# Kernel optimization log

Hardware: AMD Instinct MI355X
Metric: run time of the kernel (lower is better)

## Reference

```python
import jax, jax.numpy as jnp
import numpy as np

B, T, V, C = 4, 2048, 1024, 256
NB_L, NB_M, NB_H = 16, 32, 64


def _band_w(basis, coeffs, soft):
    # basis: (V, 2*nb), coeffs: (C, 2*nb) -> w: (V, C)
    w = basis @ coeffs.T
    return jax.nn.softmax(w, axis=0) if soft else w


def _rms_norm(x):
    eps = jnp.asarray(jnp.finfo(x.dtype).eps, x.dtype)
    return x * jax.lax.rsqrt(jnp.mean(jnp.square(x), axis=-1, keepdims=True) + eps)


def _retrieve(x, basis, qc, kc, vc, decay_logit):
    # x: (B,T,V) -> (B,T,C); decay-weighted dense T x T retrieval
    q = x @ _band_w(basis, qc, True)
    k = x @ _band_w(basis, kc, True)
    v = x @ _band_w(basis, vc, True)
    scores = jnp.einsum('btc,bsc->bts', q, k)
    decay = jax.nn.sigmoid(decay_logit)
    pos = jnp.arange(T)
    diff = pos[None, :] - pos[:, None]  # diff[i,j] = j - i (as in torch code)
    dw = (decay ** jnp.maximum(diff - 1, 0).astype(x.dtype)) * (diff > 0).astype(x.dtype)
    return jnp.einsum('bts,bsc->btc', scores * dw[None], v)


def _project(r, basis, oc, out_scale):
    return jnp.einsum('btc,vc->btv', r, basis @ oc.T) * out_scale


def _transform(x, basis, read_c, mix, bias):
    z = x @ _band_w(basis, read_c, True)
    return jax.nn.gelu(z @ mix + bias, approximate=False)


def _write_back(h, basis, write_c, out_scale):
    return jnp.einsum('btc,vc->btv', h, basis @ write_c.T) * out_scale


def setup_inputs() -> dict:
    key = jax.random.key(0)
    ks = iter(jax.random.split(key, 48))
    s = 0.02

    def rn(shape, scale=s):
        return jax.random.normal(next(ks), shape, dtype=jnp.float32) * scale

    d = {
        'x': jax.random.normal(next(ks), (B, T, V), dtype=jnp.float32),
        'basis_low': jax.random.normal(next(ks), (V, 2 * NB_L), dtype=jnp.float32),
        'basis_mid': jax.random.normal(next(ks), (V, 2 * NB_M), dtype=jnp.float32),
        'basis_high': jax.random.normal(next(ks), (V, 2 * NB_H), dtype=jnp.float32),
    }
    for pre, nb, dec in (('slow', NB_L, 4.0), ('fast', NB_H, 2.0)):
        for nm in ('q', 'k', 'v', 'o'):
            d[f'{pre}_{nm}'] = rn((C, 2 * nb))
        d[f'{pre}_decay'] = jnp.asarray(dec, jnp.float32)
        d[f'{pre}_scale'] = jnp.asarray(0.1, jnp.float32)
    for pre, nb in (('low', NB_L), ('mid', NB_M), ('high', NB_H)):
        d[f'{pre}_read'] = rn((C, 2 * nb))
        d[f'{pre}_write'] = rn((C, 2 * nb))
        d[f'{pre}_mix'] = rn((C, C))
        d[f'{pre}_bias'] = jnp.zeros((C,), jnp.float32)
        d[f'{pre}_oscale'] = jnp.asarray(0.1, jnp.float32)
    d['tg_w'] = rn((C, C)); d['tg_b'] = jnp.zeros((C,), jnp.float32)
    d['alpha_w'] = rn((C, C)); d['alpha_b'] = jnp.zeros((C,), jnp.float32)
    for nm in ('mem_slow_scale', 'mem_fast_scale', 'op_low_scale', 'op_mid_scale', 'op_high_scale'):
        d[nm] = jnp.ones((1,), jnp.float32)
    return d


def reference(x, basis_low, basis_mid, basis_high,
              slow_q, slow_k, slow_v, slow_o, slow_decay, slow_scale,
              fast_q, fast_k, fast_v, fast_o, fast_decay, fast_scale,
              low_read, low_write, low_mix, low_bias, low_oscale,
              mid_read, mid_write, mid_mix, mid_bias, mid_oscale,
              high_read, high_write, high_mix, high_bias, high_oscale,
              tg_w, tg_b, alpha_w, alpha_b,
              mem_slow_scale, mem_fast_scale, op_low_scale, op_mid_scale, op_high_scale):
    # Phase 1: temporal mixing
    xn = _rms_norm(x)
    r_slow = _retrieve(xn, basis_low, slow_q, slow_k, slow_v, slow_decay)
    r_fast = _retrieve(xn, basis_high, fast_q, fast_k, fast_v, fast_decay)
    tg = jax.nn.sigmoid(r_slow @ tg_w + tg_b)
    r_fast = tg * r_fast
    x = x + (_project(r_slow, basis_low, slow_o, slow_scale) * mem_slow_scale
             + _project(r_fast, basis_high, fast_o, fast_scale) * mem_fast_scale)
    # Phase 2: band processing
    xn = _rms_norm(x)
    h_low = _transform(xn, basis_low, low_read, low_mix, low_bias)
    h_mid = _transform(xn, basis_mid, mid_read, mid_mix, mid_bias)
    h_high = _transform(xn, basis_high, high_read, high_mix, high_bias)
    ag = jax.nn.sigmoid(h_low @ alpha_w + alpha_b)
    h_high = ag * h_high
    x = x + (_write_back(h_low, basis_low, low_write, low_oscale) * op_low_scale
             + _write_back(h_mid, basis_mid, mid_write, mid_oscale) * op_mid_scale
             + _write_back(h_high, basis_high, high_write, high_oscale) * op_high_scale)
    return x
```

## Files before the change

kernel.cpp:

```cpp
#include <hip/hip_runtime.h>
#include <math.h>

#define BB 4
#define TT 2048
#define VV 1024
#define CC 256
#define MR (BB*TT)

using short8  = __attribute__((ext_vector_type(8))) short;
using ushort8 = __attribute__((ext_vector_type(8))) unsigned short;
using f32x4   = __attribute__((ext_vector_type(4))) float;

__device__ __forceinline__ float bs2f(unsigned short s) {
    return __uint_as_float(((unsigned int)s) << 16);
}
__device__ __forceinline__ unsigned short f2bs(float f) {
    unsigned int u = __float_as_uint(f);
    u += 0x7fffu + ((u >> 16) & 1u);
    return (unsigned short)(u >> 16);
}
__device__ __forceinline__ void gl_lds16(const void* g, void* l) {
    __builtin_amdgcn_global_load_lds(
        (const __attribute__((address_space(1))) unsigned int*)g,
        (__attribute__((address_space(3))) unsigned int*)l, 16, 0, 0);
}
__device__ __forceinline__ float sigm(float x) { return 1.f / (1.f + expf(-x)); }
__device__ __forceinline__ float erf_f(float x) {
    float ax = fabsf(x);
    float t = 1.f / (1.f + 0.3275911f * ax);
    float p = t * (0.254829592f + t * (-0.284496736f + t * (1.421413741f +
              t * (-1.453152027f + t * 1.061405429f))));
    float e = 1.f - p * expf(-ax * ax);
    return copysignf(e, x);
}

struct CastJob { const float* src; unsigned short* dst; int n; };
struct CastArgs { CastJob j[17]; };

__global__ void cast_bf16_multi(CastArgs a) {
    CastJob jb = a.j[blockIdx.x];
    int off = (blockIdx.y * 256 + threadIdx.x) * 8;
    if (off + 8 > jb.n) return;
    float4 v0 = *reinterpret_cast<const float4*>(jb.src + off);
    float4 v1 = *reinterpret_cast<const float4*>(jb.src + off + 4);
    ushort8 u;
    u[0] = f2bs(v0.x); u[1] = f2bs(v0.y); u[2] = f2bs(v0.z); u[3] = f2bs(v0.w);
    u[4] = f2bs(v1.x); u[5] = f2bs(v1.y); u[6] = f2bs(v1.z); u[7] = f2bs(v1.w);
    *reinterpret_cast<ushort8*>(jb.dst + off) = u;
}

__global__ void softmax_rows(unsigned short* __restrict__ w) {
    int row = blockIdx.x * 4 + (threadIdx.x >> 6);
    int lane = threadIdx.x & 63;
    ushort4* rp = reinterpret_cast<ushort4*>(w + (size_t)row * 1024);
    float v[16];
    #pragma unroll
    for (int i = 0; i < 4; ++i) {
        ushort4 u = rp[lane + i * 64];
        v[i*4+0] = bs2f(u.x); v[i*4+1] = bs2f(u.y);
        v[i*4+2] = bs2f(u.z); v[i*4+3] = bs2f(u.w);
    }
    float m = v[0];
    #pragma unroll
    for (int i = 1; i < 16; ++i) m = fmaxf(m, v[i]);
    #pragma unroll
    for (int o = 32; o > 0; o >>= 1) m = fmaxf(m, __shfl_xor(m, o));
    float s = 0.f;
    #pragma unroll
    for (int i = 0; i < 16; ++i) { v[i] = expf(v[i] - m); s += v[i]; }
    #pragma unroll
    for (int o = 32; o > 0; o >>= 1) s += __shfl_xor(s, o);
    float inv = 1.f / s;
    #pragma unroll
    for (int i = 0; i < 4; ++i) {
        ushort4 u;
        u.x = f2bs(v[i*4+0] * inv); u.y = f2bs(v[i*4+1] * inv);
        u.z = f2bs(v[i*4+2] * inv); u.w = f2bs(v[i*4+3] * inv);
        rp[lane + i * 64] = u;
    }
}

__global__ void prep_T5(const float* s0, const float* s1, const float* s2,
                        const float* s3, const float* s4,
                        unsigned short* d0, unsigned short* d1, unsigned short* d2,
                        unsigned short* d3, unsigned short* d4) {
    int y = blockIdx.y;
    const float* W = y == 0 ? s0 : y == 1 ? s1 : y == 2 ? s2 : y == 3 ? s3 : s4;
    unsigned short* WT = y == 0 ? d0 : y == 1 ? d1 : y == 2 ? d2 : y == 3 ? d3 : d4;
    int n = blockIdx.x, k = threadIdx.x;
    WT[(size_t)n * 256 + k] = f2bs(W[(size_t)k * 256 + n]);
}

__global__ void rmsnorm_k(const float* __restrict__ x, unsigned short* __restrict__ xn) {
    int row = blockIdx.x * 4 + (threadIdx.x >> 6);
    int lane = threadIdx.x & 63;
    const float4* src = reinterpret_cast<const float4*>(x + (size_t)row * VV);
    float4 v[4];
    float s = 0.f;
    #pragma unroll
    for (int i = 0; i < 4; ++i) {
        v[i] = src[lane + i * 64];
        s += v[i].x*v[i].x + v[i].y*v[i].y + v[i].z*v[i].z + v[i].w*v[i].w;
    }
    #pragma unroll
    for (int o = 32; o > 0; o >>= 1) s += __shfl_xor(s, o);
    float r = rsqrtf(s * (1.f / VV) + 1.1920929e-7f);
    ushort4* dst = reinterpret_cast<ushort4*>(xn + (size_t)row * VV);
    #pragma unroll
    for (int i = 0; i < 4; ++i) {
        ushort4 u;
        u.x = f2bs(v[i].x * r); u.y = f2bs(v[i].y * r);
        u.z = f2bs(v[i].z * r); u.w = f2bs(v[i].w * r);
        dst[lane + i * 64] = u;
    }
}

__global__ void transpose4_k(const unsigned short* __restrict__ qkv,
                             unsigned short* __restrict__ vt_s,
                             unsigned short* __restrict__ vt_f,
                             unsigned short* __restrict__ kts_s,
                             unsigned short* __restrict__ kts_f,
                             const float* __restrict__ dls,
                             const float* __restrict__ dlf) {
    __shared__ unsigned short tile[32][33];
    int z = blockIdx.z, b = z & 3, which = z >> 2;
    int srcoff = which == 0 ? 512 : which == 1 ? 1280 : which == 2 ? 256 : 1024;
    unsigned short* dst = which == 0 ? vt_s : which == 1 ? vt_f : which == 2 ? kts_s : kts_f;
    float l2d = 0.f;
    if (which == 2) l2d = log2f(sigm(dls[0]));
    if (which == 3) l2d = log2f(sigm(dlf[0]));
    int t0 = blockIdx.x * 32, c0 = blockIdx.y * 32;
    int tx = threadIdx.x & 31, ty = threadIdx.x >> 5;
    const unsigned short* src = qkv + srcoff;
    #pragma unroll
    for (int i = 0; i < 4; ++i) {
        int r = ty + i * 8;
        tile[r][tx] = src[(size_t)(b * TT + t0 + r) * 1536 + c0 + tx];
    }
    __syncthreads();
    float w = (which >= 2) ? exp2f(l2d * (float)((t0 + tx) & 127)) : 1.f;
    #pragma unroll
    for (int i = 0; i < 4; ++i) {
        int r = ty + i * 8;
        dst[((size_t)b * CC + c0 + r) * TT + t0 + tx] = f2bs(bs2f(tile[tx][r]) * w);
    }
}

__device__ __forceinline__ void gemm64_core(
    const unsigned short* A, int lda, const unsigned short* Bt, int ldb,
    int K, int m0, int n0, short8* As, short8* Bs, f32x4 (&acc)[2][2]) {
    const int tid = threadIdx.x;
    const int lane = tid & 63, wid = tid >> 6;
    const int wm = wid >> 1, wn = wid & 1;
    const int lrow = tid >> 2, lch = tid & 3;
    const int sws = lch ^ ((lrow >> 1) & 3);
    const unsigned short* ag = A + (size_t)(m0 + lrow) * lda + lch * 8;
    const unsigned short* bg = Bt + (size_t)(n0 + lrow) * ldb + lch * 8;
    #pragma unroll
    for (int i = 0; i < 2; ++i)
        #pragma unroll
        for (int j = 0; j < 2; ++j) acc[i][j] = {0.f, 0.f, 0.f, 0.f};
    const int g = lane >> 4;
    const int ra0 = wm * 32 + (lane & 15);
    const int rb0 = wn * 32 + (lane & 15);
    for (int k0 = 0; k0 < K; k0 += 32) {
        As[lrow * 4 + sws] = *reinterpret_cast<const short8*>(ag + k0);
        Bs[lrow * 4 + sws] = *reinterpret_cast<const short8*>(bg + k0);
        __syncthreads();
        short8 af[2], bf[2];
        #pragma unroll
        for (int i = 0; i < 2; ++i) {
            int ra = ra0 + i * 16;
            af[i] = As[ra * 4 + (g ^ ((ra >> 1) & 3))];
            int rb = rb0 + i * 16;
            bf[i] = Bs[rb * 4 + (g ^ ((rb >> 1) & 3))];
        }
        #pragma unroll
        for (int i = 0; i < 2; ++i)
            #pragma unroll
            for (int j = 0; j < 2; ++j)
                acc[i][j] = __builtin_amdgcn_mfma_f32_16x16x32_bf16(af[i], bf[j], acc[i][j], 0, 0, 0);
        __syncthreads();
    }
}

#define EPI_LOOP(MV, NV, VV_, BODY)                                            \
    {   const int lane_ = threadIdx.x & 63, wid_ = threadIdx.x >> 6;           \
        const int wm_ = wid_ >> 1, wn_ = wid_ & 1;                             \
        _Pragma("unroll")                                                      \
        for (int i_ = 0; i_ < 2; ++i_)                                         \
        { _Pragma("unroll")                                                    \
          for (int j_ = 0; j_ < 2; ++j_)                                       \
          { _Pragma("unroll")                                                  \
            for (int r_ = 0; r_ < 4; ++r_)                                     \
            { int MV = m0 + wm_ * 32 + i_ * 16 + (lane_ >> 4) * 4 + r_;        \
              int NV = n0 + wn_ * 32 + j_ * 16 + (lane_ & 15);                 \
              float VV_ = acc[i_][j_][r_];                                     \
              BODY } } } }

struct MJob {
    const unsigned short* A; const unsigned short* Bt; unsigned short* outb;
    const float* s1; const float* s2;
    int lda, ldb, K, ldo, gx, nblk;
};
struct MJobs5 { MJob j[5]; };

template<int EPI>
__global__ __launch_bounds__(256)
void gemm_multi_k(MJobs5 js) {
    int bid = blockIdx.x, ji = 0, base = 0;
    while (bid >= base + js.j[ji].nblk) { base += js.j[ji].nblk; ++ji; }
    MJob jb = js.j[ji];
    int rem = bid - base;
    int m0 = (rem / jb.gx) * 64, n0 = (rem % jb.gx) * 64;
    __shared__ short8 As[256], Bs[256];
    f32x4 acc[2][2];
    gemm64_core(jb.A, jb.lda, jb.Bt, jb.ldb, jb.K, m0, n0, As, Bs, acc);
    float sc = 1.f;
    if constexpr (EPI == 4) sc = jb.s1[0] * jb.s2[0];
    EPI_LOOP(m, n, v, { jb.outb[(size_t)m * jb.ldo + n] = f2bs(v * sc); })
}

__global__ __launch_bounds__(256)
void sig_k(const unsigned short* A, int lda, const unsigned short* Bt,
           const float* bias, const unsigned short* aux, int ldaux,
           unsigned short* outb, int ldo, int coloff) {
    int m0 = blockIdx.y * 64, n0 = blockIdx.x * 64;
    __shared__ short8 As[256], Bs[256];
    f32x4 acc[2][2];
    gemm64_core(A, lda, Bt, 256, 256, m0, n0, As, Bs, acc);
    EPI_LOOP(m, n, v, {
        float s = sigm(v + bias[n]);
        float a = bs2f(aux[(size_t)m * ldaux + n]);
        outb[(size_t)m * ldo + coloff + n] = f2bs(s * a);
    })
}

__global__ __launch_bounds__(256)
void gelu3_k(const unsigned short* zbuf, const unsigned short* WT_mix,
             const float* lb, const float* mb, const float* hb,
             unsigned short* hcat, unsigned short* hhigh) {
    int zi = blockIdx.z;
    const unsigned short* A = zbuf + zi * 256;
    const unsigned short* Bt = WT_mix + (size_t)zi * 65536;
    const float* bias = zi == 0 ? lb : zi == 1 ? mb : hb;
    unsigned short* outb = zi == 2 ? hhigh : hcat;
    int ldo = zi == 2 ? 256 : 768;
    int coloff = zi == 1 ? 256 : 0;
    int m0 = blockIdx.y * 64, n0 = blockIdx.x * 64;
    __shared__ short8 As[256], Bs[256];
    f32x4 acc[2][2];
    gemm64_core(A, 768, Bt, 256, 256, m0, n0, As, Bs, acc);
    EPI_LOOP(m, n, v, {
        float z = v + bias[n];
        float h = 0.5f * z * (1.f + erf_f(z * 0.70710678118654752f));
        outb[(size_t)m * ldo + coloff + n] = f2bs(h);
    })
}

struct EpiP {
    float* outf; const float* addf;
    unsigned short* outb; int ldo;
    const unsigned short* A2; const unsigned short* B2;
    float* outf2;
    unsigned short* outb2; int ldo2;
    const float* dls; const float* dlf;
};

template<int EPI, int BATCH>
__global__ __launch_bounds__(256)
void gemm128_k(const unsigned short* __restrict__ A, int lda,
               const unsigned short* __restrict__ Bt, int ldb, int K, EpiP ep) {
    __shared__ short8 As[1024], Bs[1024];
    const int tid = threadIdx.x;
    const int lane = tid & 63, wid = tid >> 6;
    const int wm = wid >> 1, wn = wid & 1;

    int sel = 0, z2v = 0, zb = 0, zp = 0;
    if constexpr (BATCH == 1) {
        int zz = blockIdx.z; sel = zz >> 6; z2v = zz & 63;
        zb = z2v >> 4; zp = z2v & 15;
        if (sel) { A = ep.A2; Bt = ep.B2; }
        A  += (size_t)(zb * CC) * lda + zp * 128;
        Bt += (size_t)(zb * CC) * ldb + zp * 128;
    } else if constexpr (BATCH == 2) {
        int zz = blockIdx.z; sel = zz >= 60 ? 1 : 0; z2v = sel ? zz - 60 : zz;
        zb = z2v / 15; zp = z2v % 15;
        if (sel) Bt = ep.B2;
        A  += (sel ? 768 : 0) + (size_t)(zb * TT + zp * 128) * lda;
        Bt += (size_t)z2v * 65536;
    }

    int lin = blockIdx.y * gridDim.x + blockIdx.x;
    int ngw = gridDim.x * gridDim.y;
    int sw = lin;
    if (!(ngw & 7)) sw = (lin & 7) * (ngw >> 3) + (lin >> 3);
    const int m0 = (sw / gridDim.x) * 128, n0 = (sw % gridDim.x) * 128;

    const int srow = lane >> 3, schk = (lane & 7) ^ srow;
    const unsigned short* ga = A + (size_t)(m0 + wid * 32 + srow) * lda + schk * 8;
    const unsigned short* gb = Bt + (size_t)(n0 + wid * 32 + srow) * ldb + schk * 8;
    short8* lA = &As[(wid * 32) * 8];
    short8* lB = &Bs[(wid * 32) * 8];

    const int fr = lane & 15, fg = lane >> 4;

    f32x4 acc[4][4];
    #pragma unroll
    for (int i = 0; i < 4; ++i)
        #pragma unroll
        for (int j = 0; j < 4; ++j) acc[i][j] = {0.f, 0.f, 0.f, 0.f};

    for (int k0 = 0; k0 < K; k0 += 64) {
        #pragma unroll
        for (int q = 0; q < 4; ++q) {
            gl_lds16(ga + (size_t)(q * 8) * lda + k0, lA + q * 64);
            gl_lds16(gb + (size_t)(q * 8) * ldb + k0, lB + q * 64);
        }
        __syncthreads();
        #pragma unroll
        for (int kk = 0; kk < 2; ++kk) {
            short8 af[4], bf[4];
            #pragma unroll
            for (int i = 0; i < 4; ++i) {
                int ra = wm * 64 + i * 16 + fr;
                af[i] = As[ra * 8 + ((kk * 4 + fg) ^ (ra & 7))];
                int rb = wn * 64 + i * 16 + fr;
                bf[i] = Bs[rb * 8 + ((kk * 4 + fg) ^ (rb & 7))];
            }
            #pragma unroll
            for (int i = 0; i < 4; ++i)
                #pragma unroll
                for (int j = 0; j < 4; ++j)
                    acc[i][j] = __builtin_amdgcn_mfma_f32_16x16x32_bf16(af[i], bf[j], acc[i][j], 0, 0, 0);
        }
        __syncthreads();
    }

    float l2d6 = 0.f;
    if constexpr (EPI == 6) l2d6 = log2f(sigm(sel ? ep.dlf[0] : ep.dls[0]));
    unsigned short* ob = ep.outb;
    int ldo = ep.ldo;
    if constexpr (EPI == 6) { if (sel) { ob = ep.outb2; ldo = ep.ldo2; } }
    float* gout = nullptr;
    if constexpr (EPI == 5) gout = (sel ? ep.outf2 : ep.outf) + (size_t)z2v * 65536;

    #pragma unroll
    for (int i = 0; i < 4; ++i) {
        #pragma unroll
        for (int j = 0; j < 4; ++j) {
            #pragma unroll
            for (int r = 0; r < 4; ++r) {
                int m = m0 + wm * 64 + i * 16 + fg * 4 + r;
                int n = n0 + wn * 64 + j * 16 + fr;
                float v = acc[i][j][r];
                if constexpr (EPI == 0) {
                    ob[(size_t)m * ldo + n] = f2bs(v);
                } else if constexpr (EPI == 3) {
                    size_t idx = (size_t)m * ep.ldo + n;
                    ep.outf[idx] = ep.addf[idx] + v;
                } else if constexpr (EPI == 5) {
                    gout[(size_t)m * 256 + n] = v;
                } else if constexpr (EPI == 6) {
                    float rs = exp2f(l2d6 * (float)(127 - m));
                    size_t idx = (size_t)(zb * TT + zp * 128 + m) * ldo + n;
                    ob[idx] = f2bs(bs2f(ob[idx]) + v * rs);
                }
            }
        }
    }
}

__global__ __launch_bounds__(256)
void attn_k(const unsigned short* __restrict__ qkv,
            const unsigned short* __restrict__ vt_s,
            const unsigned short* __restrict__ vt_f,
            const float* __restrict__ dls, const float* __restrict__ dlf,
            unsigned short* __restrict__ rcat, unsigned short* __restrict__ rfast) {
    int y = blockIdx.y;
    int qoff = y ? 768 : 0, koff = y ? 1024 : 256;
    const unsigned short* vt = y ? vt_f : vt_s;
    unsigned short* rout = y ? rfast : rcat;
    int ldr = y ? 256 : 512;
    float l2d = log2f(sigm(y ? dlf[0] : dls[0]));

    int blk = blockIdx.x;
    int b = blk >> 7;
    int t0 = (blk & 127) << 4;
    int tid = threadIdx.x;
    int lane = tid & 63, wid = tid >> 6;

    __shared__ short8 Pl[4][64];
    __shared__ float  red[16][260];

    short8 qf[8];
    const size_t rowq = (size_t)(b * TT + t0 + (lane & 15)) * 1536 + qoff + (lane >> 4) * 8;
    #pragma unroll
    for (int ch = 0; ch < 8; ++ch)
        qf[ch] = *reinterpret_cast<const short8*>(qkv + rowq + ch * 32);

    f32x4 racc[16];
    #pragma unroll
    for (int i = 0; i < 16; ++i) racc[i] = {0.f, 0.f, 0.f, 0.f};

    unsigned short* pb = reinterpret_cast<unsigned short*>(&Pl[wid][0]);

    int sBeg = t0 & ~31;
    int sEnd = (t0 & ~127) + 128;
    const int tl = (lane >> 4) * 4;

    for (int s0 = sBeg + wid * 32; s0 < sEnd; s0 += 128) {
        #pragma unroll
        for (int h = 0; h < 2; ++h) {
            f32x4 sacc = {0.f, 0.f, 0.f, 0.f};
            const unsigned short* kb =
                qkv + (size_t)(b * TT + s0 + h * 16 + (lane & 15)) * 1536 + koff + (lane >> 4) * 8;
            #pragma unroll
            for (int ch = 0; ch < 8; ++ch) {
                short8 kf = *reinterpret_cast<const short8*>(kb + ch * 32);
                sacc = __builtin_amdgcn_mfma_f32_16x16x32_bf16(qf[ch], kf, sacc, 0, 0, 0);
            }
            int scol = s0 + h * 16 + (lane & 15);
            #pragma unroll
            for (int r = 0; r < 4; ++r) {
                int trow = t0 + tl + r;
                int d = scol - trow;
                float w = (d > 0) ? exp2f(l2d * (float)(d - 1)) : 0.f;
                int prow = tl + r, pcol = h * 16 + (lane & 15);
                int swp = (pcol >> 3) ^ ((prow >> 1) & 3);
                pb[(prow * 4 + swp) * 8 + (pcol & 7)] = f2bs(sacc[r] * w);
            }
        }
        asm volatile("s_waitcnt lgkmcnt(0)" ::: "memory");
        __builtin_amdgcn_sched_barrier(0);
        short8 pf;
        { int prow = lane & 15; pf = Pl[wid][prow * 4 + ((lane >> 4) ^ ((prow >> 1) & 3))]; }
        const unsigned short* vb = vt + ((size_t)b * CC + (lane & 15)) * TT + s0 + (lane >> 4) * 8;
        #pragma unroll
        for (int nt = 0; nt < 16; ++nt) {
            short8 vf = *reinterpret_cast<const short8*>(vb + (size_t)nt * 16 * TT);
            racc[nt] = __builtin_amdgcn_mfma_f32_16x16x32_bf16(pf, vf, racc[nt], 0, 0, 0);
        }
    }

    for (int w = 0; w < 4; ++w) {
        if (wid == w) {
            #pragma unroll
            for (int nt = 0; nt < 16; ++nt)
                #pragma unroll
                for (int r = 0; r < 4; ++r) {
                    int row = tl + r, col = nt * 16 + (lane & 15);
                    if (w == 0) red[row][col] = racc[nt][r];
                    else        red[row][col] += racc[nt][r];
                }
        }
        __syncthreads();
    }

    {
        int row = tid >> 4, c0 = (tid & 15) * 16;
        ushort8 lo, hi;
        #pragma unroll
        for (int j = 0; j < 8; ++j) lo[j] = f2bs(red[row][c0 + j]);
        #pragma unroll
        for (int j = 0; j < 8; ++j) hi[j] = f2bs(red[row][c0 + 8 + j]);
        unsigned short* dst = rout + (size_t)(b * TT + t0 + row) * ldr + c0;
        *reinterpret_cast<ushort8*>(dst)     = lo;
        *reinterpret_cast<ushort8*>(dst + 8) = hi;
    }
}

__global__ void scan_states2(const float* __restrict__ Gs, const float* __restrict__ Gf,
                             const float* __restrict__ dls, const float* __restrict__ dlf,
                             unsigned short* __restrict__ STs, unsigned short* __restrict__ STf) {
    int sel = blockIdx.z;
    const float* G = sel ? Gf : Gs;
    unsigned short* ST = sel ? STf : STs;
    float d = sigm(sel ? dlf[0] : dls[0]);
    int b = blockIdx.y;
    int e0 = (blockIdx.x * 256 + threadIdx.x) * 4;
    float dL = exp2f(log2f(d) * 128.f);
    float4 s = {0.f, 0.f, 0.f, 0.f};
    for (int c = 15; c >= 1; --c) {
        float4 g = *reinterpret_cast<const float4*>(G + (((size_t)(b * 16 + c)) << 16) + e0);
        s.x = g.x + dL * s.x; s.y = g.y + dL * s.y;
        s.z = g.z + dL * s.z; s.w = g.w + dL * s.w;
        ushort4 o;
        o.x = f2bs(s.x); o.y = f2bs(s.y); o.z = f2bs(s.z); o.w = f2bs(s.w);
        *reinterpret_cast<ushort4*>(ST + (((size_t)(b * 15 + c - 1)) << 16) + e0) = o;
    }
}

extern "C" void kernel_launch(void* const* d_in, const int* in_sizes, int n_in,
                              void* d_out, int out_size, void* d_ws, size_t ws_size,
                              hipStream_t stream) {
    (void)in_sizes; (void)n_in; (void)out_size; (void)ws_size;
    const float* x          = (const float*)d_in[0];
    const float* basis_low  = (const float*)d_in[1];
    const float* basis_mid  = (const float*)d_in[2];
    const float* basis_high = (const float*)d_in[3];
    const float* slow_q = (const float*)d_in[4];
    const float* slow_k = (const float*)d_in[5];
    const float* slow_v = (const float*)d_in[6];
    const float* slow_o = (const float*)d_in[7];
    const float* slow_decay = (const float*)d_in[8];
    const float* slow_scale = (const float*)d_in[9];
    const float* fast_q = (const float*)d_in[10];
    const float* fast_k = (const float*)d_in[11];
    const float* fast_v = (const float*)d_in[12];
    const float* fast_o = (const float*)d_in[13];
    const float* fast_decay = (const float*)d_in[14];
    const float* fast_scale = (const float*)d_in[15];
    const float* low_read  = (const float*)d_in[16];
    const float* low_write = (const float*)d_in[17];
    const float* low_mix   = (const float*)d_in[18];
    const float* low_bias  = (const float*)d_in[19];
    const float* low_oscale= (const float*)d_in[20];
    const float* mid_read  = (const float*)d_in[21];
    const float* mid_write = (const float*)d_in[22];
    const float* mid_mix   = (const float*)d_in[23];
    const float* mid_bias  = (const float*)d_in[24];
    const float* mid_oscale= (const float*)d_in[25];
    const float* high_read  = (const float*)d_in[26];
    const float* high_write = (const float*)d_in[27];
    const float* high_mix   = (const float*)d_in[28];
    const float* high_bias  = (const float*)d_in[29];
    const float* high_oscale= (const float*)d_in[30];
    const float* tg_w    = (const float*)d_in[31];
    const float* tg_b    = (const float*)d_in[32];
    const float* alpha_w = (const float*)d_in[33];
    const float* alpha_b = (const float*)d_in[34];
    const float* mem_slow_scale = (const float*)d_in[35];
    const float* mem_fast_scale = (const float*)d_in[36];
    const float* op_low_scale   = (const float*)d_in[37];
    const float* op_mid_scale   = (const float*)d_in[38];
    const float* op_high_scale  = (const float*)d_in[39];
    float* out = (float*)d_out;

    char* ws = (char*)d_ws;
    size_t off = 0;
    auto alloc = [&](size_t n) { char* p = ws + off; off += (n + 255) & ~(size_t)255; return p; };
    unsigned short* WT_p1   = (unsigned short*)alloc((size_t)6 * CC * VV * 2);
    unsigned short* WT_read = (unsigned short*)alloc((size_t)3 * CC * VV * 2);
    unsigned short* Wcat_o  = (unsigned short*)alloc((size_t)VV * 512 * 2);
    unsigned short* Wcat_w  = (unsigned short*)alloc((size_t)VV * 768 * 2);
    unsigned short* WT_mix  = (unsigned short*)alloc((size_t)3 * 65536 * 2);
    unsigned short* WT_tg   = (unsigned short*)alloc((size_t)65536 * 2);
    unsigned short* WT_al   = (unsigned short*)alloc((size_t)65536 * 2);
    unsigned short* bb_low  = (unsigned short*)alloc((size_t)VV * 32 * 2);
    unsigned short* bb_mid  = (unsigned short*)alloc((size_t)VV * 64 * 2);
    unsigned short* bb_high = (unsigned short*)alloc((size_t)VV * 128 * 2);
    unsigned short* cqkv_l  = (unsigned short*)alloc((size_t)768 * 32 * 2);
    unsigned short* cqkv_h  = (unsigned short*)alloc((size_t)768 * 128 * 2);
    unsigned short* crd_l   = (unsigned short*)alloc((size_t)256 * 32 * 2);
    unsigned short* crd_m   = (unsigned short*)alloc((size_t)256 * 64 * 2);
    unsigned short* crd_h   = (unsigned short*)alloc((size_t)256 * 128 * 2);
    unsigned short* cO_s    = (unsigned short*)alloc((size_t)256 * 32 * 2);
    unsigned short* cO_f    = (unsigned short*)alloc((size_t)256 * 128 * 2);
    unsigned short* cW_l    = (unsigned short*)alloc((size_t)256 * 32 * 2);
    unsigned short* cW_m    = (unsigned short*)alloc((size_t)256 * 64 * 2);
    unsigned short* cW_h    = (unsigned short*)alloc((size_t)256 * 128 * 2);
    unsigned short* xn      = (unsigned short*)alloc((size_t)MR * VV * 2);
    unsigned short* qkv     = (unsigned short*)alloc((size_t)MR * 1536 * 2);
    unsigned short* vt_s    = (unsigned short*)alloc((size_t)BB * CC * TT * 2);
    unsigned short* vt_f    = (unsigned short*)alloc((size_t)BB * CC * TT * 2);
    unsigned short* kts_s   = (unsigned short*)alloc((size_t)BB * CC * TT * 2);
    unsigned short* kts_f   = (unsigned short*)alloc((size_t)BB * CC * TT * 2);
    unsigned short* ST_s    = (unsigned short*)alloc((size_t)BB * 15 * 65536 * 2);
    unsigned short* ST_f    = (unsigned short*)alloc((size_t)BB * 15 * 65536 * 2);
    unsigned short* rcat    = (unsigned short*)alloc((size_t)MR * 512 * 2);
    unsigned short* rfast   = (unsigned short*)alloc((size_t)MR * CC * 2);
    unsigned short* hhigh   = (unsigned short*)alloc((size_t)MR * CC * 2);
    float* Gs = (float*)xn;
    float* Gf = (float*)rcat;
    unsigned short* z    = qkv;
    unsigned short* hcat = qkv + (size_t)MR * 768;

    {
        CastArgs ca;
        int i = 0;
        auto J = [&](const float* s, unsigned short* d, int n) { ca.j[i].src = s; ca.j[i].dst = d; ca.j[i].n = n; ++i; };
        J(basis_low,  bb_low,  VV * 32);
        J(basis_mid,  bb_mid,  VV * 64);
        J(basis_high, bb_high, VV * 128);
        J(slow_q, cqkv_l + 0 * 256 * 32, 256 * 32);
        J(slow_k, cqkv_l + 1 * 256 * 32, 256 * 32);
        J(slow_v, cqkv_l + 2 * 256 * 32, 256 * 32);
        J(fast_q, cqkv_h + 0 * 256 * 128, 256 * 128);
        J(fast_k, cqkv_h + 1 * 256 * 128, 256 * 128);
        J(fast_v, cqkv_h + 2 * 256 * 128, 256 * 128);
        J(low_read,  crd_l, 256 * 32);
        J(mid_read,  crd_m, 256 * 64);
        J(high_read, crd_h, 256 * 128);
        J(slow_o,    cO_s,  256 * 32);
        J(fast_o,    cO_f,  256 * 128);
        J(low_write, cW_l,  256 * 32);
        J(mid_write, cW_m,  256 * 64);
        J(high_write,cW_h,  256 * 128);
        cast_bf16_multi<<<dim3(17, 64), 256, 0, stream>>>(ca);
    }

    {
        MJobs5 js;
        auto S = [&](int i, const unsigned short* A, int lda, const unsigned short* B, int K,
                     unsigned short* o, int nb) {
            js.j[i].A = A; js.j[i].Bt = B; js.j[i].outb = o; js.j[i].s1 = nullptr; js.j[i].s2 = nullptr;
            js.j[i].lda = lda; js.j[i].ldb = K; js.j[i].K = K; js.j[i].ldo = VV; js.j[i].gx = 16; js.j[i].nblk = nb;
        };
        S(0, cqkv_l, 32,  bb_low,  32,  WT_p1,                    192);
        S(1, cqkv_h, 128, bb_high, 128, WT_p1 + (size_t)768 * VV, 192);
        S(2, crd_l,  32,  bb_low,  32,  WT_read,                   64);
        S(3, crd_m,  64,  bb_mid,  64,  WT_read + (size_t)256 * VV, 64);
        S(4, crd_h,  128, bb_high, 128, WT_read + (size_t)512 * VV, 64);
        gemm_multi_k<0><<<576, 256, 0, stream>>>(js);
    }
    softmax_rows<<<576, 256, 0, stream>>>(WT_p1);

    {
        MJobs5 js;
        auto S = [&](int i, const unsigned short* A, int lda, const unsigned short* B, int K,
                     unsigned short* o, int ldo, const float* s1, const float* s2) {
            js.j[i].A = A; js.j[i].Bt = B; js.j[i].outb = o; js.j[i].s1 = s1; js.j[i].s2 = s2;
            js.j[i].lda = lda; js.j[i].ldb = K; js.j[i].K = K; js.j[i].ldo = ldo; js.j[i].gx = 4; js.j[i].nblk = 64;
        };
        S(0, bb_low,  32,  cO_s, 32,  Wcat_o,       512, slow_scale,  mem_slow_scale);
        S(1, bb_high, 128, cO_f, 128, Wcat_o + 256, 512, fast_scale,  mem_fast_scale);
        S(2, bb_low,  32,  cW_l, 32,  Wcat_w,       768, low_oscale,  op_low_scale);
        S(3, bb_mid,  64,  cW_m, 64,  Wcat_w + 256, 768, mid_oscale,  op_mid_scale);
        S(4, bb_high, 128, cW_h, 128, Wcat_w + 512, 768, high_oscale, op_high_scale);
        gemm_multi_k<4><<<320, 256, 0, stream>>>(js);
    }

    prep_T5<<<dim3(256, 5), 256, 0, stream>>>(tg_w, alpha_w, low_mix, mid_mix, high_mix,
                                              WT_tg, WT_al, WT_mix, WT_mix + 65536, WT_mix + 131072);

    rmsnorm_k<<<MR / 4, 256, 0, stream>>>(x, xn);
    { EpiP ep{}; ep.outb = qkv; ep.ldo = 1536;
      gemm128_k<0,0><<<dim3(12, 64), 256, 0, stream>>>(xn, 1024, WT_p1, 1024, 1024, ep); }
    transpose4_k<<<dim3(64, 8, 16), 256, 0, stream>>>(qkv, vt_s, vt_f, kts_s, kts_f, slow_decay, fast_decay);
    { EpiP ep{}; ep.outf = Gs; ep.outf2 = Gf; ep.A2 = vt_f; ep.B2 = kts_f;
      gemm128_k<5,1><<<dim3(2, 2, 128), 256, 0, stream>>>(vt_s, TT, kts_s, TT, 128, ep); }
    scan_states2<<<dim3(64, 4, 2), 256, 0, stream>>>(Gs, Gf, slow_decay, fast_decay, ST_s, ST_f);
    attn_k<<<dim3(512, 2), 256, 0, stream>>>(qkv, vt_s, vt_f, slow_decay, fast_decay, rcat, rfast);
    { EpiP ep{}; ep.outb = rcat; ep.ldo = 512; ep.outb2 = rfast; ep.ldo2 = 256;
      ep.dls = slow_decay; ep.dlf = fast_decay; ep.B2 = ST_f;
      gemm128_k<6,2><<<dim3(2, 1, 120), 256, 0, stream>>>(qkv, 1536, ST_s, 256, 256, ep); }
    sig_k<<<dim3(4, 128), 256, 0, stream>>>(rcat, 512, WT_tg, tg_b, rfast, 256, rcat, 512, 256);
    { EpiP ep{}; ep.outf = out; ep.addf = x; ep.ldo = 1024;
      gemm128_k<3,0><<<dim3(8, 64), 256, 0, stream>>>(rcat, 512, Wcat_o, 512, 512, ep); }

    rmsnorm_k<<<MR / 4, 256, 0, stream>>>(out, xn);
    { EpiP ep{}; ep.outb = z; ep.ldo = 768;
      gemm128_k<0,0><<<dim3(6, 64), 256, 0, stream>>>(xn, 1024, WT_read, 1024, 1024, ep); }
    gelu3_k<<<dim3(4, 128, 3), 256, 0, stream>>>(z, WT_mix, low_bias, mid_bias, high_bias, hcat, hhigh);
    sig_k<<<dim3(4, 128), 256, 0, stream>>>(hcat, 768, WT_al, alpha_b, hhigh, 256, hcat, 768, 512);
    { EpiP ep{}; ep.outf = out; ep.addf = out; ep.ldo = 1024;
      gemm128_k<3,0><<<dim3(6, 64), 256, 0, stream>>>(hcat, 768, Wcat_w, 768, 768, ep); }
}
```

Before: 274.8 us.

## Fuse inter-chunk state contribution into attention kernel and merge weight-prep GEMM launches

The separate GEMM that added each 128-row chunk's carried state (query times scanned state, with decay rescale) into rcat/rfast is removed. Its work now runs inside attn_k, which initializes its accumulators from the state product before the intra-chunk loop. This drops one launch and a read-modify-write pass over the bf16 outputs. The two weight-prep multi-GEMM launches are also merged into one 10-job launch with a runtime scale check. In exchange, attn_k does more per-block work and reads state fragments straight from global memory.

```diff
diff --git a/kernel.cpp b/kernel.cpp
--- a/kernel.cpp
+++ b/kernel.cpp
@@ -203,11 +203,10 @@
     const float* s1; const float* s2;
     int lda, ldb, K, ldo, gx, nblk;
 };
-struct MJobs5 { MJob j[5]; };
-
-template<int EPI>
+struct MJobs10 { MJob j[10]; };
+
 __global__ __launch_bounds__(256)
-void gemm_multi_k(MJobs5 js) {
+void gemm_multi_k(MJobs10 js) {
     int bid = blockIdx.x, ji = 0, base = 0;
     while (bid >= base + js.j[ji].nblk) { base += js.j[ji].nblk; ++ji; }
     MJob jb = js.j[ji];
@@ -216,8 +215,7 @@
     __shared__ short8 As[256], Bs[256];
     f32x4 acc[2][2];
     gemm64_core(jb.A, jb.lda, jb.Bt, jb.ldb, jb.K, m0, n0, As, Bs, acc);
-    float sc = 1.f;
-    if constexpr (EPI == 4) sc = jb.s1[0] * jb.s2[0];
+    float sc = jb.s1 ? jb.s1[0] * jb.s2[0] : 1.f;
     EPI_LOOP(m, n, v, { jb.outb[(size_t)m * jb.ldo + n] = f2bs(v * sc); })
 }
 
@@ -263,8 +261,6 @@
     unsigned short* outb; int ldo;
     const unsigned short* A2; const unsigned short* B2;
     float* outf2;
-    unsigned short* outb2; int ldo2;
-    const float* dls; const float* dlf;
 };
 
 template<int EPI, int BATCH>
@@ -276,19 +272,13 @@
     const int lane = tid & 63, wid = tid >> 6;
     const int wm = wid >> 1, wn = wid & 1;
 
-    int sel = 0, z2v = 0, zb = 0, zp = 0;
+    int sel = 0, z2v = 0;
     if constexpr (BATCH == 1) {
         int zz = blockIdx.z; sel = zz >> 6; z2v = zz & 63;
-        zb = z2v >> 4; zp = z2v & 15;
+        int zb = z2v >> 4, zp = z2v & 15;
         if (sel) { A = ep.A2; Bt = ep.B2; }
         A  += (size_t)(zb * CC) * lda + zp * 128;
         Bt += (size_t)(zb * CC) * ldb + zp * 128;
-    } else if constexpr (BATCH == 2) {
-        int zz = blockIdx.z; sel = zz >= 60 ? 1 : 0; z2v = sel ? zz - 60 : zz;
-        zb = z2v / 15; zp = z2v % 15;
-        if (sel) Bt = ep.B2;
-        A  += (sel ? 768 : 0) + (size_t)(zb * TT + zp * 128) * lda;
-        Bt += (size_t)z2v * 65536;
     }
 
     int lin = blockIdx.y * gridDim.x + blockIdx.x;
@@ -337,11 +327,6 @@
         __syncthreads();
     }
 
-    float l2d6 = 0.f;
-    if constexpr (EPI == 6) l2d6 = log2f(sigm(sel ? ep.dlf[0] : ep.dls[0]));
-    unsigned short* ob = ep.outb;
-    int ldo = ep.ldo;
-    if constexpr (EPI == 6) { if (sel) { ob = ep.outb2; ldo = ep.ldo2; } }
     float* gout = nullptr;
     if constexpr (EPI == 5) gout = (sel ? ep.outf2 : ep.outf) + (size_t)z2v * 65536;
 
@@ -355,16 +340,12 @@
                 int n = n0 + wn * 64 + j * 16 + fr;
                 float v = acc[i][j][r];
                 if constexpr (EPI == 0) {
-                    ob[(size_t)m * ldo + n] = f2bs(v);
+                    ep.outb[(size_t)m * ep.ldo + n] = f2bs(v);
                 } else if constexpr (EPI == 3) {
                     size_t idx = (size_t)m * ep.ldo + n;
                     ep.outf[idx] = ep.addf[idx] + v;
-                } else if constexpr (EPI == 5) {
+                } else {
                     gout[(size_t)m * 256 + n] = v;
-                } else if constexpr (EPI == 6) {
-                    float rs = exp2f(l2d6 * (float)(127 - m));
-                    size_t idx = (size_t)(zb * TT + zp * 128 + m) * ldo + n;
-                    ob[idx] = f2bs(bs2f(ob[idx]) + v * rs);
                 }
             }
         }
@@ -375,6 +356,8 @@
 void attn_k(const unsigned short* __restrict__ qkv,
             const unsigned short* __restrict__ vt_s,
             const unsigned short* __restrict__ vt_f,
+            const unsigned short* __restrict__ ST_s,
+            const unsigned short* __restrict__ ST_f,
             const float* __restrict__ dls, const float* __restrict__ dlf,
             unsigned short* __restrict__ rcat, unsigned short* __restrict__ rfast) {
     int y = blockIdx.y;
@@ -403,11 +386,33 @@
     #pragma unroll
     for (int i = 0; i < 16; ++i) racc[i] = {0.f, 0.f, 0.f, 0.f};
 
+    const int tl = (lane >> 4) * 4;
+
+    int p = (t0 >> 7) & 15;
+    if (p < 15) {
+        const unsigned short* stb = (y ? ST_f : ST_s)
+            + (((size_t)(b * 15 + p)) << 16)
+            + (size_t)(lane & 15) * 256 + (lane >> 4) * 8;
+        #pragma unroll
+        for (int kc2 = 0; kc2 < 2; ++kc2) {
+            int kc = wid * 2 + kc2;
+            #pragma unroll
+            for (int nt = 0; nt < 16; ++nt) {
+                short8 stf = *reinterpret_cast<const short8*>(stb + (size_t)nt * 16 * 256 + kc * 32);
+                racc[nt] = __builtin_amdgcn_mfma_f32_16x16x32_bf16(qf[kc], stf, racc[nt], 0, 0, 0);
+            }
+        }
+        float base = (float)(127 - ((t0 & 127) + tl));
+        #pragma unroll
+        for (int nt = 0; nt < 16; ++nt)
+            #pragma unroll
+            for (int r = 0; r < 4; ++r)
+                racc[nt][r] *= exp2f(l2d * (base - (float)r));
+    }
+
     unsigned short* pb = reinterpret_cast<unsigned short*>(&Pl[wid][0]);
-
     int sBeg = t0 & ~31;
     int sEnd = (t0 & ~127) + 128;
-    const int tl = (lane >> 4) * 4;
 
     for (int s0 = sBeg + wid * 32; s0 < sEnd; s0 += 128) {
         #pragma unroll
@@ -601,35 +606,26 @@
     }
 
     {
-        MJobs5 js;
+        MJobs10 js;
         auto S = [&](int i, const unsigned short* A, int lda, const unsigned short* B, int K,
-                     unsigned short* o, int nb) {
-            js.j[i].A = A; js.j[i].Bt = B; js.j[i].outb = o; js.j[i].s1 = nullptr; js.j[i].s2 = nullptr;
-            js.j[i].lda = lda; js.j[i].ldb = K; js.j[i].K = K; js.j[i].ldo = VV; js.j[i].gx = 16; js.j[i].nblk = nb;
+                     unsigned short* o, int ldo, int gx, int nb,
+                     const float* s1, const float* s2) {
+            js.j[i].A = A; js.j[i].Bt = B; js.j[i].outb = o; js.j[i].s1 = s1; js.j[i].s2 = s2;
+            js.j[i].lda = lda; js.j[i].ldb = K; js.j[i].K = K; js.j[i].ldo = ldo; js.j[i].gx = gx; js.j[i].nblk = nb;
         };
-        S(0, cqkv_l, 32,  bb_low,  32,  WT_p1,                    192);
-        S(1, cqkv_h, 128, bb_high, 128, WT_p1 + (size_t)768 * VV, 192);
-        S(2, crd_l,  32,  bb_low,  32,  WT_read,                   64);
-        S(3, crd_m,  64,  bb_mid,  64,  WT_read + (size_t)256 * VV, 64);
-        S(4, crd_h,  128, bb_high, 128, WT_read + (size_t)512 * VV, 64);
-        gemm_multi_k<0><<<576, 256, 0, stream>>>(js);
+        S(0, cqkv_l, 32,  bb_low,  32,  WT_p1,                     VV, 16, 192, nullptr, nullptr);
+        S(1, cqkv_h, 128, bb_high, 128, WT_p1 + (size_t)768 * VV,  VV, 16, 192, nullptr, nullptr);
+        S(2, crd_l,  32,  bb_low,  32,  WT_read,                    VV, 16, 64, nullptr, nullptr);
+        S(3, crd_m,  64,  bb_mid,  64,  WT_read + (size_t)256 * VV, VV, 16, 64, nullptr, nullptr);
+        S(4, crd_h,  128, bb_high, 128, WT_read + (size_t)512 * VV, VV, 16, 64, nullptr, nullptr);
+        S(5, bb_low,  32,  cO_s, 32,  Wcat_o,       512, 4, 64, slow_scale,  mem_slow_scale);
+        S(6, bb_high, 128, cO_f, 128, Wcat_o + 256, 512, 4, 64, fast_scale,  mem_fast_scale);
+        S(7, bb_low,  32,  cW_l, 32,  Wcat_w,       768, 4, 64, low_oscale,  op_low_scale);
+        S(8, bb_mid,  64,  cW_m, 64,  Wcat_w + 256, 768, 4, 64, mid_oscale,  op_mid_scale);
+        S(9, bb_high, 128, cW_h, 128, Wcat_w + 512, 768, 4, 64, high_oscale, op_high_scale);
+        gemm_multi_k<<<896, 256, 0, stream>>>(js);
     }
     softmax_rows<<<576, 256, 0, stream>>>(WT_p1);
-
-    {
-        MJobs5 js;
-        auto S = [&](int i, const unsigned short* A, int lda, const unsigned short* B, int K,
-                     unsigned short* o, int ldo, const float* s1, const float* s2) {
-            js.j[i].A = A; js.j[i].Bt = B; js.j[i].outb = o; js.j[i].s1 = s1; js.j[i].s2 = s2;
-            js.j[i].lda = lda; js.j[i].ldb = K; js.j[i].K = K; js.j[i].ldo = ldo; js.j[i].gx = 4; js.j[i].nblk = 64;
-        };
-        S(0, bb_low,  32,  cO_s, 32,  Wcat_o,       512, slow_scale,  mem_slow_scale);
-        S(1, bb_high, 128, cO_f, 128, Wcat_o + 256, 512, fast_scale,  mem_fast_scale);
-        S(2, bb_low,  32,  cW_l, 32,  Wcat_w,       768, low_oscale,  op_low_scale);
-        S(3, bb_mid,  64,  cW_m, 64,  Wcat_w + 256, 768, mid_oscale,  op_mid_scale);
-        S(4, bb_high, 128, cW_h, 128, Wcat_w + 512, 768, high_oscale, op_high_scale);
-        gemm_multi_k<4><<<320, 256, 0, stream>>>(js);
-    }
 
     prep_T5<<<dim3(256, 5), 256, 0, stream>>>(tg_w, alpha_w, low_mix, mid_mix, high_mix,
                                               WT_tg, WT_al, WT_mix, WT_mix + 65536, WT_mix + 131072);
@@ -641,10 +637,8 @@
     { EpiP ep{}; ep.outf = Gs; ep.outf2 = Gf; ep.A2 = vt_f; ep.B2 = kts_f;
       gemm128_k<5,1><<<dim3(2, 2, 128), 256, 0, stream>>>(vt_s, TT, kts_s, TT, 128, ep); }
     scan_states2<<<dim3(64, 4, 2), 256, 0, stream>>>(Gs, Gf, slow_decay, fast_decay, ST_s, ST_f);
-    attn_k<<<dim3(512, 2), 256, 0, stream>>>(qkv, vt_s, vt_f, slow_decay, fast_decay, rcat, rfast);
-    { EpiP ep{}; ep.outb = rcat; ep.ldo = 512; ep.outb2 = rfast; ep.ldo2 = 256;
-      ep.dls = slow_decay; ep.dlf = fast_decay; ep.B2 = ST_f;
-      gemm128_k<6,2><<<dim3(2, 1, 120), 256, 0, stream>>>(qkv, 1536, ST_s, 256, 256, ep); }
+    attn_k<<<dim3(512, 2), 256, 0, stream>>>(qkv, vt_s, vt_f, ST_s, ST_f,
+                                             slow_decay, fast_decay, rcat, rfast);
     sig_k<<<dim3(4, 128), 256, 0, stream>>>(rcat, 512, WT_tg, tg_b, rfast, 256, rcat, 512, 256);
     { EpiP ep{}; ep.outf = out; ep.addf = x; ep.ldo = 1024;
       gemm128_k<3,0><<<dim3(8, 64), 256, 0, stream>>>(rcat, 512, Wcat_o, 512, 512, ep); }
```

Result: slower. 291.5 us (+6.1%).
